# Performance work log

Hardware: AMD Instinct MI355X
Metric: run time of the kernel (lower is better)

## Reference

```python
import jax, jax.numpy as jnp
import numpy as np

WINDOW = (2, 7, 7)
NUM_HEADS = 4
DIM = 128


def _relative_position_index(ws):
    d, h, w = ws
    coords = np.stack(np.meshgrid(np.arange(d), np.arange(h), np.arange(w), indexing='ij'))  # (3,d,h,w)
    cf = coords.reshape(3, -1)  # (3, N)
    rel = cf[:, :, None] - cf[:, None, :]  # (3, N, N)
    rel = rel.transpose(1, 2, 0).astype(np.int64)
    rel[:, :, 0] += d - 1
    rel[:, :, 1] += h - 1
    rel[:, :, 2] += w - 1
    rel[:, :, 0] *= (2 * h - 1) * (2 * w - 1)
    rel[:, :, 1] *= 2 * w - 1
    return rel.sum(-1).astype(np.int32)  # (N, N)


def setup_inputs() -> dict:
    key = jax.random.key(0)
    ks = jax.random.split(key, 6)
    N = WINDOW[0] * WINDOW[1] * WINDOW[2]  # 98
    B_, nW, C = 4096, 64, DIM
    x = jax.random.normal(ks[0], (B_, N, C), dtype=jnp.float32)
    mask = jax.random.normal(ks[1], (nW, N, N), dtype=jnp.float32)
    qkv_w = jax.random.normal(ks[2], (3 * C, C), dtype=jnp.float32) * (C ** -0.5)
    proj_w = jax.random.normal(ks[3], (C, C), dtype=jnp.float32) * (C ** -0.5)
    proj_b = jax.random.normal(ks[4], (C,), dtype=jnp.float32) * 0.02
    n_bias = (2 * WINDOW[0] - 1) * (2 * WINDOW[1] - 1) * (2 * WINDOW[2] - 1)  # 507
    bias_table = jax.random.normal(ks[5], (n_bias, NUM_HEADS), dtype=jnp.float32) * 0.02
    rel_index = jnp.asarray(_relative_position_index(WINDOW))
    return {"x": x, "mask": mask, "qkv_w": qkv_w, "proj_w": proj_w,
            "proj_b": proj_b, "bias_table": bias_table, "rel_index": rel_index}


def reference(x, mask, qkv_w, proj_w, proj_b, bias_table, rel_index):
    B_, N, C = x.shape
    H = NUM_HEADS
    hd = C // H
    scale = hd ** -0.5
    # qkv projection (no bias), split heads -> (3, B_, H, N, hd)
    qkv = (x @ qkv_w.T).reshape(B_, N, 3, H, hd).transpose(2, 0, 3, 1, 4)
    q, k, v = qkv[0] * scale, qkv[1], qkv[2]
    attn = jnp.einsum('bhnd,bhmd->bhnm', q, k)  # (B_, H, N, N)
    # gathered relative position bias -> (H, N, N)
    bias = bias_table[rel_index.reshape(-1)].reshape(N, N, H).transpose(2, 0, 1)
    attn = attn + bias[None]
    nW = mask.shape[0]
    attn = attn.reshape(B_ // nW, nW, H, N, N) + mask[None, :, None]
    attn = jax.nn.softmax(attn.reshape(B_, H, N, N), axis=-1)
    out = jnp.einsum('bhnm,bhmd->bhnd', attn, v)  # (B_, H, N, hd)
    out = out.transpose(0, 2, 1, 3).reshape(B_, N, C)
    return out @ proj_w.T + proj_b
```

## Files before the change

### kernel.cpp

```cpp
#include <hip/hip_runtime.h>

typedef __attribute__((ext_vector_type(8))) short bf8;
typedef __attribute__((ext_vector_type(4))) float f4;
typedef __attribute__((ext_vector_type(16))) float f16v;
typedef __attribute__((ext_vector_type(2))) unsigned int u32x2;
typedef __attribute__((ext_vector_type(4))) unsigned int u32x4;

#define MFMA16(A,B,C) __builtin_amdgcn_mfma_f32_16x16x32_bf16(A,B,C,0,0,0)
#define MFMA32(A,B,C) __builtin_amdgcn_mfma_f32_32x32x16_bf16(A,B,C,0,0,0)

#define NTOK 98
#define SROW 136
#define SCALE 0.17677669529663687f

__device__ __forceinline__ unsigned short bfu(float f) {
  union { float f; unsigned u; } un; un.f = f;
  unsigned r = un.u + 0x7FFFu + ((un.u >> 16) & 1u);
  return (unsigned short)(r >> 16);
}
__device__ __forceinline__ unsigned cvtpk(float a, float b) {
  unsigned r;
  asm("v_cvt_pk_bf16_f32 %0, %1, %2" : "=v"(r) : "v"(a), "v"(b));
  return r;
}

__global__ void prep_kernel(const float* __restrict__ qkv_w,
                            const float* __restrict__ proj_w,
                            const float* __restrict__ bias_table,
                            const int* __restrict__ rel_index,
                            const float* __restrict__ mask,
                            unsigned short* __restrict__ wq,
                            unsigned short* __restrict__ wp,
                            float* __restrict__ bsmall,
                            float* __restrict__ bm, int use_bm) {
  const int T1 = 384*128, T2 = T1 + 128*128;
  const int TS = 4*128*112;
  const int T3 = T2 + TS;
  const int TB = 64*4*128*112;
  const int total = T3 + (use_bm ? TB : 0);
  for (int idx = blockIdx.x*blockDim.x + threadIdx.x; idx < total;
       idx += gridDim.x*blockDim.x) {
    if (idx < T1)      wq[idx] = bfu(qkv_w[idx]);
    else if (idx < T2) wp[idx - T1] = bfu(proj_w[idx - T1]);
    else if (idx < T3) {
      int t = idx - T2;
      int m = t % 112, n = (t/112) & 127, h = t / (112*128);
      float v;
      if (m >= NTOK)      v = -1e30f;
      else if (n >= NTOK) v = 0.f;
      else                v = bias_table[rel_index[n*98+m]*4 + h];
      bsmall[t] = v;
    } else {
      int t = idx - T3;
      int m = t % 112; int r = t / 112;
      int n = r & 127; r >>= 7;
      int h = r & 3;   int w = r >> 2;
      float v;
      if (m >= NTOK)      v = -1e30f;
      else if (n >= NTOK) v = 0.f;
      else v = bias_table[rel_index[n*98+m]*4 + h] + mask[(size_t)w*9604 + n*98 + m];
      bm[t] = v;
    }
  }
}

template<int USE_BM>
__launch_bounds__(1024, 1)
__global__ void wattn_kernel(const float* __restrict__ x,
                             const float* __restrict__ mask,
                             const float* __restrict__ proj_b,
                             const unsigned short* __restrict__ wqkv,
                             const unsigned short* __restrict__ wproj,
                             const float* __restrict__ bsmall,
                             const float* __restrict__ bm,
                             float* __restrict__ out) {
  __shared__ unsigned short xb[128*SROW];
  __shared__ unsigned short qb[128*SROW];
  __shared__ unsigned short kb[128*SROW];
  __shared__ unsigned short vt[128*SROW];

  const int b = blockIdx.x, tid = threadIdx.x;
  const int wid = tid >> 6, lane = tid & 63;
  const int g = lane >> 4, c = lane & 15;

  for (int i = tid; i < 14*SROW; i += 1024) xb[98*SROW + i] = 0;
  for (int i = tid; i < 16*SROW; i += 1024) { qb[112*SROW + i] = 0; kb[112*SROW + i] = 0; }

  const float* xp = x + (size_t)b * (NTOK*128);
  for (int i = tid; i < (NTOK*128)/4; i += 1024) {
    float4 v4 = ((const float4*)xp)[i];
    int e = i*4, n = e >> 7, cc = e & 127;
    u32x2 u; u[0] = cvtpk(v4.x, v4.y); u[1] = cvtpk(v4.z, v4.w);
    *(u32x2*)&xb[n*SROW + cc] = u;
  }
  __syncthreads();

  for (int k3 = 0; k3 < 3; ++k3) {
    const int u = wid + 16*k3;
    const int ot = u >> 1, half = u & 1;
    const int ib = half ? 4 : 0, ni = half ? 3 : 4;
    if (ot < 16) {
      const unsigned short* wptr = wqkv + (size_t)(ot*16 + c)*128;
      f4 acc[4] = {};
      #pragma unroll
      for (int kk = 0; kk < 4; ++kk) {
        bf8 wf = *(const bf8*)(wptr + kk*32 + g*8);
        #pragma unroll
        for (int i = 0; i < 4; ++i) if (i < ni) {
          bf8 xf = *(const bf8*)(&xb[((ib+i)*16 + c)*SROW + kk*32 + g*8]);
          acc[i] = MFMA16(wf, xf, acc[i]);
        }
      }
      unsigned short* dst = (ot < 8) ? qb : kb;
      const int col = (ot & 7)*16 + g*4;
      const float sc = (ot < 8) ? SCALE : 1.f;
      #pragma unroll
      for (int i = 0; i < 4; ++i) if (i < ni) {
        u32x2 uu;
        uu[0] = cvtpk(acc[i][0]*sc, acc[i][1]*sc);
        uu[1] = cvtpk(acc[i][2]*sc, acc[i][3]*sc);
        *(u32x2*)&dst[((ib+i)*16 + c)*SROW + col] = uu;
      }
    } else {
      const int ov = ot - 16;
      const unsigned short* wptr = wqkv + (size_t)(256 + ov*16 + c)*128;
      f4 acc[4] = {};
      #pragma unroll
      for (int kk = 0; kk < 4; ++kk) {
        bf8 wf = *(const bf8*)(wptr + kk*32 + g*8);
        #pragma unroll
        for (int i = 0; i < 4; ++i) if (i < ni) {
          bf8 xf = *(const bf8*)(&xb[((ib+i)*16 + c)*SROW + kk*32 + g*8]);
          acc[i] = MFMA16(xf, wf, acc[i]);
        }
      }
      #pragma unroll
      for (int i = 0; i < 4; ++i) if (i < ni) {
        u32x2 uu;
        uu[0] = cvtpk(acc[i][0], acc[i][1]);
        uu[1] = cvtpk(acc[i][2], acc[i][3]);
        *(u32x2*)&vt[(ov*16 + c)*SROW + (ib+i)*16 + g*4] = uu;
      }
    }
  }
  __syncthreads();

  {
    const int hh = wid & 3, i32 = wid >> 2;
    const int l31 = lane & 31, hl = lane >> 5;
    const int n = i32*32 + l31;

    f16v sj[4];
    const float* bmp = USE_BM ? (bm + ((size_t)((b & 63)*4 + hh)*128 + n)*112)
                              : (bsmall + ((size_t)hh*128 + n)*112);
    #pragma unroll
    for (int j = 0; j < 4; ++j)
      #pragma unroll
      for (int a = 0; a < 4; ++a) {
        f4 t;
        if (j == 3 && a >= 2) t = (f4){-1e30f, -1e30f, -1e30f, -1e30f};
        else t = *(const f4*)(bmp + j*32 + a*8 + hl*4);
        sj[j][4*a+0] = t[0]; sj[j][4*a+1] = t[1];
        sj[j][4*a+2] = t[2]; sj[j][4*a+3] = t[3];
      }
    if (!USE_BM && n < NTOK) {
      const float* mw = mask + (size_t)(b & 63)*9604 + n*98;
      #pragma unroll
      for (int j = 0; j < 4; ++j)
        #pragma unroll
        for (int a = 0; a < 4; ++a) {
          if (j == 3 && a >= 2) continue;
          #pragma unroll
          for (int bb = 0; bb < 4; ++bb) {
            int m = j*32 + a*8 + hl*4 + bb;
            if (m < NTOK) sj[j][4*a+bb] += mw[m];
          }
        }
    }
    #pragma unroll
    for (int kd = 0; kd < 2; ++kd) {
      bf8 qf = *(const bf8*)(&qb[n*SROW + hh*32 + kd*16 + hl*8]);
      #pragma unroll
      for (int j = 0; j < 4; ++j) {
        bf8 kf = *(const bf8*)(&kb[(j*32 + l31)*SROW + hh*32 + kd*16 + hl*8]);
        sj[j] = MFMA32(kf, qf, sj[j]);
      }
    }
    float sum = 0.f;
    #pragma unroll
    for (int j = 0; j < 4; ++j)
      #pragma unroll
      for (int r = 0; r < 16; ++r) { float e = __expf(sj[j][r]); sj[j][r] = e; sum += e; }
    sum += __shfl_xor(sum, 32);
    const float inv = 1.f / sum;
    unsigned P2[4][4][2];
    #pragma unroll
    for (int j = 0; j < 4; ++j)
      #pragma unroll
      for (int a = 0; a < 4; ++a) {
        P2[j][a][0] = cvtpk(sj[j][4*a+0], sj[j][4*a+1]);
        P2[j][a][1] = cvtpk(sj[j][4*a+2], sj[j][4*a+3]);
      }
    f16v acc = {0.f,0.f,0.f,0.f,0.f,0.f,0.f,0.f,0.f,0.f,0.f,0.f,0.f,0.f,0.f,0.f};
    #pragma unroll
    for (int km = 0; km < 7; ++km) {
      const int j = km >> 1, a0 = 2*(km & 1);
      bf8 vf = *(const bf8*)(&vt[(hh*32 + l31)*SROW + km*16 + hl*8]);
      unsigned o0 = P2[j][a0][0],   o1 = P2[j][a0][1];
      unsigned o2 = P2[j][a0+1][0], o3 = P2[j][a0+1][1];
      unsigned s0 = __shfl_xor(o0, 32), s1 = __shfl_xor(o1, 32);
      unsigned s2 = __shfl_xor(o2, 32), s3 = __shfl_xor(o3, 32);
      u32x4 pw;
      pw[0] = hl ? s2 : o0;  pw[1] = hl ? s3 : o1;
      pw[2] = hl ? o2 : s0;  pw[3] = hl ? o3 : s1;
      acc = MFMA32(vf, *(bf8*)&pw, acc);
    }
    #pragma unroll
    for (int a = 0; a < 4; ++a) {
      u32x2 uu;
      uu[0] = cvtpk(acc[4*a+0]*inv, acc[4*a+1]*inv);
      uu[1] = cvtpk(acc[4*a+2]*inv, acc[4*a+3]*inv);
      *(u32x2*)&xb[n*SROW + hh*32 + a*8 + hl*4] = uu;
    }
  }
  __syncthreads();

  for (int k3 = 0; k3 < 4; ++k3) {
    const int t = wid + 16*k3;
    if (t < 56) {
      const int i = t >> 3, ot = t & 7;
      const unsigned short* wptr = wproj + (size_t)(ot*16 + c)*128;
      f4 acc = {0.f, 0.f, 0.f, 0.f};
      #pragma unroll
      for (int kk = 0; kk < 4; ++kk) {
        bf8 wf = *(const bf8*)(wptr + kk*32 + g*8);
        bf8 xf = *(const bf8*)(&xb[(i*16 + c)*SROW + kk*32 + g*8]);
        acc = MFMA16(wf, xf, acc);
      }
      const int n2 = i*16 + c;
      if (n2 < NTOK) {
        f4 pb4 = *(const f4*)(proj_b + ot*16 + g*4);
        f4 o4 = {acc[0]+pb4[0], acc[1]+pb4[1], acc[2]+pb4[2], acc[3]+pb4[3]};
        *(f4*)(out + (size_t)b*(NTOK*128) + n2*128 + ot*16 + g*4) = o4;
      }
    }
  }
}

extern "C" void kernel_launch(void* const* d_in, const int* in_sizes, int n_in,
                              void* d_out, int out_size, void* d_ws, size_t ws_size,
                              hipStream_t stream) {
  const float* x          = (const float*)d_in[0];
  const float* mask       = (const float*)d_in[1];
  const float* qkv_w      = (const float*)d_in[2];
  const float* proj_w     = (const float*)d_in[3];
  const float* proj_b     = (const float*)d_in[4];
  const float* bias_table = (const float*)d_in[5];
  const int*   rel_index  = (const int*)d_in[6];

  unsigned short* wq = (unsigned short*)d_ws;
  unsigned short* wp = wq + 384*128;
  float* bsmall = (float*)((char*)d_ws + 131072);
  float* bm     = (float*)((char*)d_ws + 360448);

  const size_t need = 360448u + (size_t)64*4*128*112*4;
  const int use_bm = (ws_size >= need) ? 1 : 0;

  prep_kernel<<<2048, 256, 0, stream>>>(qkv_w, proj_w, bias_table, rel_index, mask,
                                        wq, wp, bsmall, bm, use_bm);
  if (use_bm)
    wattn_kernel<1><<<4096, 1024, 0, stream>>>(x, mask, proj_b, wq, wp, bsmall, bm,
                                               (float*)d_out);
  else
    wattn_kernel<0><<<4096, 1024, 0, stream>>>(x, mask, proj_b, wq, wp, bsmall, bm,
                                               (float*)d_out);
}
```

Measured before the change: 295.0 us.

## Store combined bias+mask in fp16 and fold log2e into scale for exp2

The precomputed bias+mask table is stored as fp16 instead of fp32, halving its footprint and global reads. log2(e) is folded into the query scale and bias so softmax can use exp2f directly. The bias add is moved after the QK MFMA and fused with the exponent, so accumulators start at zero. Padded rows are zeroed explicitly instead of carrying -1e30 sentinels. fp16 storage of bias+mask adds some rounding error to the logits.

```diff
diff --git a/kernel.cpp b/kernel.cpp
--- a/kernel.cpp
+++ b/kernel.cpp
@@ -11,7 +11,8 @@
 
 #define NTOK 98
 #define SROW 136
-#define SCALE 0.17677669529663687f
+#define LOG2E 1.4426950408889634f
+#define QSCALE (0.17677669529663687f * LOG2E)
 
 __device__ __forceinline__ unsigned short bfu(float f) {
   union { float f; unsigned u; } un; un.f = f;
@@ -22,6 +23,9 @@
   unsigned r;
   asm("v_cvt_pk_bf16_f32 %0, %1, %2" : "=v"(r) : "v"(a), "v"(b));
   return r;
+}
+__device__ __forceinline__ float h2f(unsigned short u) {
+  return (float)__builtin_bit_cast(_Float16, u);
 }
 
 __global__ void prep_kernel(const float* __restrict__ qkv_w,
@@ -32,7 +36,7 @@
                             unsigned short* __restrict__ wq,
                             unsigned short* __restrict__ wp,
                             float* __restrict__ bsmall,
-                            float* __restrict__ bm, int use_bm) {
+                            unsigned short* __restrict__ bmh, int use_bm) {
   const int T1 = 384*128, T2 = T1 + 128*128;
   const int TS = 4*128*112;
   const int T3 = T2 + TS;
@@ -48,7 +52,7 @@
       float v;
       if (m >= NTOK)      v = -1e30f;
       else if (n >= NTOK) v = 0.f;
-      else                v = bias_table[rel_index[n*98+m]*4 + h];
+      else                v = bias_table[rel_index[n*98+m]*4 + h] * LOG2E;
       bsmall[t] = v;
     } else {
       int t = idx - T3;
@@ -58,8 +62,8 @@
       float v;
       if (m >= NTOK)      v = -1e30f;
       else if (n >= NTOK) v = 0.f;
-      else v = bias_table[rel_index[n*98+m]*4 + h] + mask[(size_t)w*9604 + n*98 + m];
-      bm[t] = v;
+      else v = (bias_table[rel_index[n*98+m]*4 + h] + mask[(size_t)w*9604 + n*98 + m]) * LOG2E;
+      bmh[t] = __builtin_bit_cast(unsigned short, (_Float16)v);
     }
   }
 }
@@ -72,7 +76,7 @@
                              const unsigned short* __restrict__ wqkv,
                              const unsigned short* __restrict__ wproj,
                              const float* __restrict__ bsmall,
-                             const float* __restrict__ bm,
+                             const unsigned short* __restrict__ bmh,
                              float* __restrict__ out) {
   __shared__ unsigned short xb[128*SROW];
   __shared__ unsigned short qb[128*SROW];
@@ -82,6 +86,9 @@
   const int b = blockIdx.x, tid = threadIdx.x;
   const int wid = tid >> 6, lane = tid & 63;
   const int g = lane >> 4, c = lane & 15;
+  const int hh = wid & 3, i32 = wid >> 2;
+  const int l31 = lane & 31, hl = lane >> 5;
+  const int nA = i32*32 + l31;
 
   for (int i = tid; i < 14*SROW; i += 1024) xb[98*SROW + i] = 0;
   for (int i = tid; i < 16*SROW; i += 1024) { qb[112*SROW + i] = 0; kb[112*SROW + i] = 0; }
@@ -89,9 +96,9 @@
   const float* xp = x + (size_t)b * (NTOK*128);
   for (int i = tid; i < (NTOK*128)/4; i += 1024) {
     float4 v4 = ((const float4*)xp)[i];
-    int e = i*4, n = e >> 7, cc = e & 127;
+    int e = i*4, nn = e >> 7, cc = e & 127;
     u32x2 u; u[0] = cvtpk(v4.x, v4.y); u[1] = cvtpk(v4.z, v4.w);
-    *(u32x2*)&xb[n*SROW + cc] = u;
+    *(u32x2*)&xb[nn*SROW + cc] = u;
   }
   __syncthreads();
 
@@ -113,7 +120,7 @@
       }
       unsigned short* dst = (ot < 8) ? qb : kb;
       const int col = (ot & 7)*16 + g*4;
-      const float sc = (ot < 8) ? SCALE : 1.f;
+      const float sc = (ot < 8) ? QSCALE : 1.f;
       #pragma unroll
       for (int i = 0; i < 4; ++i) if (i < ni) {
         u32x2 uu;
@@ -146,51 +153,60 @@
   __syncthreads();
 
   {
-    const int hh = wid & 3, i32 = wid >> 2;
-    const int l31 = lane & 31, hl = lane >> 5;
-    const int n = i32*32 + l31;
-
-    f16v sj[4];
-    const float* bmp = USE_BM ? (bm + ((size_t)((b & 63)*4 + hh)*128 + n)*112)
-                              : (bsmall + ((size_t)hh*128 + n)*112);
-    #pragma unroll
-    for (int j = 0; j < 4; ++j)
-      #pragma unroll
-      for (int a = 0; a < 4; ++a) {
-        f4 t;
-        if (j == 3 && a >= 2) t = (f4){-1e30f, -1e30f, -1e30f, -1e30f};
-        else t = *(const f4*)(bmp + j*32 + a*8 + hl*4);
-        sj[j][4*a+0] = t[0]; sj[j][4*a+1] = t[1];
-        sj[j][4*a+2] = t[2]; sj[j][4*a+3] = t[3];
-      }
-    if (!USE_BM && n < NTOK) {
-      const float* mw = mask + (size_t)(b & 63)*9604 + n*98;
+    const f16v z16 = {0.f,0.f,0.f,0.f,0.f,0.f,0.f,0.f,0.f,0.f,0.f,0.f,0.f,0.f,0.f,0.f};
+    f16v sj[4]; sj[0] = z16; sj[1] = z16; sj[2] = z16; sj[3] = z16;
+    #pragma unroll
+    for (int kd = 0; kd < 2; ++kd) {
+      bf8 qf = *(const bf8*)&qb[nA*SROW + hh*32 + kd*16 + hl*8];
+      #pragma unroll
+      for (int j = 0; j < 4; ++j) {
+        bf8 kf = *(const bf8*)&kb[(j*32 + l31)*SROW + hh*32 + kd*16 + hl*8];
+        sj[j] = MFMA32(kf, qf, sj[j]);
+      }
+    }
+    float sum = 0.f;
+    if (USE_BM) {
+      const unsigned short* bp = bmh + ((size_t)((b & 63)*4 + hh)*128 + nA)*112;
       #pragma unroll
       for (int j = 0; j < 4; ++j)
         #pragma unroll
         for (int a = 0; a < 4; ++a) {
-          if (j == 3 && a >= 2) continue;
+          if (j == 3 && a >= 2) {
+            sj[j][4*a+0] = 0.f; sj[j][4*a+1] = 0.f;
+            sj[j][4*a+2] = 0.f; sj[j][4*a+3] = 0.f;
+            continue;
+          }
+          ushort4 u = *(const ushort4*)(bp + j*32 + a*8 + hl*4);
+          float e0 = exp2f(sj[j][4*a+0] + h2f(u.x));
+          float e1 = exp2f(sj[j][4*a+1] + h2f(u.y));
+          float e2 = exp2f(sj[j][4*a+2] + h2f(u.z));
+          float e3 = exp2f(sj[j][4*a+3] + h2f(u.w));
+          sj[j][4*a+0] = e0; sj[j][4*a+1] = e1;
+          sj[j][4*a+2] = e2; sj[j][4*a+3] = e3;
+          sum += (e0 + e1) + (e2 + e3);
+        }
+    } else {
+      const float* bs = bsmall + ((size_t)hh*128 + nA)*112;
+      const float* mw = mask + (size_t)(b & 63)*9604 + (size_t)(nA < NTOK ? nA : 0)*98;
+      #pragma unroll
+      for (int j = 0; j < 4; ++j)
+        #pragma unroll
+        for (int a = 0; a < 4; ++a) {
+          if (j == 3 && a >= 2) {
+            sj[j][4*a+0] = 0.f; sj[j][4*a+1] = 0.f;
+            sj[j][4*a+2] = 0.f; sj[j][4*a+3] = 0.f;
+            continue;
+          }
           #pragma unroll
           for (int bb = 0; bb < 4; ++bb) {
             int m = j*32 + a*8 + hl*4 + bb;
-            if (m < NTOK) sj[j][4*a+bb] += mw[m];
+            float add = bs[j*32 + a*8 + hl*4 + bb];
+            if (nA < NTOK && m < NTOK) add += mw[m] * LOG2E;
+            float e = exp2f(sj[j][4*a+bb] + add);
+            sj[j][4*a+bb] = e; sum += e;
           }
         }
     }
-    #pragma unroll
-    for (int kd = 0; kd < 2; ++kd) {
-      bf8 qf = *(const bf8*)(&qb[n*SROW + hh*32 + kd*16 + hl*8]);
-      #pragma unroll
-      for (int j = 0; j < 4; ++j) {
-        bf8 kf = *(const bf8*)(&kb[(j*32 + l31)*SROW + hh*32 + kd*16 + hl*8]);
-        sj[j] = MFMA32(kf, qf, sj[j]);
-      }
-    }
-    float sum = 0.f;
-    #pragma unroll
-    for (int j = 0; j < 4; ++j)
-      #pragma unroll
-      for (int r = 0; r < 16; ++r) { float e = __expf(sj[j][r]); sj[j][r] = e; sum += e; }
     sum += __shfl_xor(sum, 32);
     const float inv = 1.f / sum;
     unsigned P2[4][4][2];
@@ -201,11 +217,11 @@
         P2[j][a][0] = cvtpk(sj[j][4*a+0], sj[j][4*a+1]);
         P2[j][a][1] = cvtpk(sj[j][4*a+2], sj[j][4*a+3]);
       }
-    f16v acc = {0.f,0.f,0.f,0.f,0.f,0.f,0.f,0.f,0.f,0.f,0.f,0.f,0.f,0.f,0.f,0.f};
+    f16v acc = z16;
     #pragma unroll
     for (int km = 0; km < 7; ++km) {
       const int j = km >> 1, a0 = 2*(km & 1);
-      bf8 vf = *(const bf8*)(&vt[(hh*32 + l31)*SROW + km*16 + hl*8]);
+      bf8 vf = *(const bf8*)&vt[(hh*32 + l31)*SROW + km*16 + hl*8];
       unsigned o0 = P2[j][a0][0],   o1 = P2[j][a0][1];
       unsigned o2 = P2[j][a0+1][0], o3 = P2[j][a0+1][1];
       unsigned s0 = __shfl_xor(o0, 32), s1 = __shfl_xor(o1, 32);
@@ -220,7 +236,7 @@
       u32x2 uu;
       uu[0] = cvtpk(acc[4*a+0]*inv, acc[4*a+1]*inv);
       uu[1] = cvtpk(acc[4*a+2]*inv, acc[4*a+3]*inv);
-      *(u32x2*)&xb[n*SROW + hh*32 + a*8 + hl*4] = uu;
+      *(u32x2*)&xb[nA*SROW + hh*32 + a*8 + hl*4] = uu;
     }
   }
   __syncthreads();
@@ -261,17 +277,17 @@
   unsigned short* wq = (unsigned short*)d_ws;
   unsigned short* wp = wq + 384*128;
   float* bsmall = (float*)((char*)d_ws + 131072);
-  float* bm     = (float*)((char*)d_ws + 360448);
-
-  const size_t need = 360448u + (size_t)64*4*128*112*4;
+  unsigned short* bmh = (unsigned short*)((char*)d_ws + 360448);
+
+  const size_t need = 360448u + (size_t)64*4*128*112*2;
   const int use_bm = (ws_size >= need) ? 1 : 0;
 
   prep_kernel<<<2048, 256, 0, stream>>>(qkv_w, proj_w, bias_table, rel_index, mask,
-                                        wq, wp, bsmall, bm, use_bm);
+                                        wq, wp, bsmall, bmh, use_bm);
   if (use_bm)
-    wattn_kernel<1><<<4096, 1024, 0, stream>>>(x, mask, proj_b, wq, wp, bsmall, bm,
+    wattn_kernel<1><<<4096, 1024, 0, stream>>>(x, mask, proj_b, wq, wp, bsmall, bmh,
                                                (float*)d_out);
   else
-    wattn_kernel<0><<<4096, 1024, 0, stream>>>(x, mask, proj_b, wq, wp, bsmall, bm,
+    wattn_kernel<0><<<4096, 1024, 0, stream>>>(x, mask, proj_b, wq, wp, bsmall, bmh,
                                                (float*)d_out);
 }
```

Result: slower. 308.9 us (+4.7%).
